# Kernel optimization log

Hardware: AMD Instinct MI355X
Metric: run time of the kernel (lower is better)

The kernel has to match this reference:

```python
import jax, jax.numpy as jnp
import numpy as np

N = 20000      # nodes
E = 320000     # edges
IN = 300       # input_channel
HID = 100      # hidden_channel (= heads*out_channels with heads=1)
R = 50         # num_relations
B = 8          # num_bases (the 4th positional arg 'heads'=8 lands on num_bases in PyG RGATConv)
HEADS = 1
CLS = 3
Q = 64         # number of query (aspect) nodes
EPS = 1e-16


def setup_inputs() -> dict:
    key = jax.random.key(0)
    ks = jax.random.split(key, 16)
    x = jax.random.normal(ks[0], (N, IN), jnp.float32)
    edge_index = jax.random.randint(ks[1], (2, E), 0, N)
    edge_type = jax.random.randint(ks[2], (E,), 0, R)
    query_indices = jax.random.randint(ks[3], (Q,), 0, N)

    def w(k, shape, scale):
        return jax.random.normal(k, shape, jnp.float32) * scale

    comp1 = w(ks[4], (R, B), 0.3)
    basis1 = w(ks[5], (B, IN, HEADS * HID), 1.0 / np.sqrt(IN))
    q1 = w(ks[6], (HEADS * HID, HEADS), 0.1)
    k1 = w(ks[7], (HEADS * HID, HEADS), 0.1)
    b1 = jnp.zeros((HEADS * HID,), jnp.float32)
    comp2 = w(ks[8], (R, B), 0.3)
    basis2 = w(ks[9], (B, HID, HEADS * HID), 1.0 / np.sqrt(HID))
    q2 = w(ks[10], (HEADS * HID, HEADS), 0.1)
    k2 = w(ks[11], (HEADS * HID, HEADS), 0.1)
    b2 = jnp.zeros((HEADS * HID,), jnp.float32)
    Wl = w(ks[12], (CLS, HID), 1.0 / np.sqrt(HID))
    bl = jnp.zeros((CLS,), jnp.float32)
    return dict(x=x, edge_index=edge_index, edge_type=edge_type,
                query_indices=query_indices,
                comp1=comp1, basis1=basis1, q1=q1, k1=k1, b1=b1,
                comp2=comp2, basis2=basis2, q2=q2, k2=k2, b2=b2,
                Wl=Wl, bl=bl)


def segment_softmax(alpha, seg, num_segments):
    # numerically-stable softmax over edges grouped by destination node
    m = jax.ops.segment_max(alpha, seg, num_segments=num_segments)  # [N, H]
    e = jnp.exp(alpha - m[seg])
    s = jax.ops.segment_sum(e, seg, num_segments=num_segments)
    return e / (s[seg] + EPS)


def rgat_conv(x, edge_index, edge_type, comp, basis, q, k, b):
    # basis-decomposed per-relation weight: [R, in, H*out]
    W = jnp.einsum('rb,bio->rio', comp, basis)
    # transform every node under every relation once, then gather per edge
    xt = jnp.einsum('ni,rio->nro', x, W)          # [N, R, H*out]
    src, dst = edge_index[0], edge_index[1]        # j -> i (source_to_target)
    xi = xt[dst, edge_type]                        # [E, H*out]
    xj = xt[src, edge_type]                        # [E, H*out]
    qi = xi @ q                                    # [E, H]
    kj = xj @ k                                    # [E, H]
    alpha = jax.nn.leaky_relu(qi + kj, 0.2)        # additive self-attention
    alpha = segment_softmax(alpha, dst, N)         # across-relation softmax
    msg = xj.reshape(E, HEADS, HID) * alpha[:, :, None]
    out = jax.ops.segment_sum(msg, dst, num_segments=N)  # [N, H, out]
    return out.reshape(N, HEADS * HID) + b         # concat=True


def reference(x, edge_index, edge_type, query_indices,
              comp1, basis1, q1, k1, b1,
              comp2, basis2, q2, k2, b2, Wl, bl):
    h = jax.nn.relu(rgat_conv(x, edge_index, edge_type, comp1, basis1, q1, k1, b1))
    h = jax.nn.relu(rgat_conv(h, edge_index, edge_type, comp2, basis2, q2, k2, b2))
    pooled = h[query_indices].mean(axis=0)          # [HID]
    return pooled @ Wl.T + bl                       # [CLS]
```

## Files before the change

### kernel.cpp

```cpp
#include <hip/hip_runtime.h>
#include <math.h>

#define N_NODES 20000
#define E_EDGES 320000
#define IN_CH   300
#define HID     100
#define R_REL   50
#define NB      8
#define CLS     3
#define NQ      64
#define OUTW    800
#define ZW      128
#define KP1     320
#define KP2     128
#define MPAD    20224
#define NPAIR   79
#define GEMM_RG 25
#define SCAN_BLKS ((N_NODES + 255) / 256)

typedef unsigned short ushort_t;
typedef __attribute__((ext_vector_type(8))) short     short8;
typedef __attribute__((ext_vector_type(8))) unsigned short ushort8;
typedef __attribute__((ext_vector_type(4))) float     f32x4;
typedef __attribute__((ext_vector_type(2))) float     f32x2;

__device__ __forceinline__ ushort_t f2bf_rne(float f) {
    unsigned u = __float_as_uint(f);
    unsigned r = (u + 0x7fffu + ((u >> 16) & 1u)) >> 16;
    return (ushort_t)r;
}
__device__ __forceinline__ float bf2f(ushort_t u) {
    return __uint_as_float((unsigned)u << 16);
}

__global__ __launch_bounds__(256) void zero_deg2(int* __restrict__ dd,
                                                 int* __restrict__ ds) {
    int i = blockIdx.x * 256 + threadIdx.x;
    if (i < N_NODES) { dd[i] = 0; ds[i] = 0; }
}

__global__ __launch_bounds__(256) void hist2_kernel(
        const int* __restrict__ ei, int* __restrict__ dd,
        int* __restrict__ ds) {
    int e = blockIdx.x * 256 + threadIdx.x;
    if (e < E_EDGES) {
        atomicAdd(&dd[ei[E_EDGES + e]], 1);
        atomicAdd(&ds[ei[e]], 1);
    }
}

__global__ __launch_bounds__(256) void scan1_both(
        const int* __restrict__ deg_d, int* __restrict__ rp_d, int* __restrict__ bsum_d,
        const int* __restrict__ deg_s, int* __restrict__ rp_s, int* __restrict__ bsum_s) {
    int set = blockIdx.x / SCAN_BLKS, blk = blockIdx.x % SCAN_BLKS;
    const int* deg = set ? deg_s : deg_d;
    int* rowptr    = set ? rp_s  : rp_d;
    int* bsum      = set ? bsum_s : bsum_d;
    __shared__ int s[256];
    int tid = threadIdx.x;
    int idx = blk * 256 + tid;
    int v = (idx < N_NODES) ? deg[idx] : 0;
    s[tid] = v; __syncthreads();
    #pragma unroll
    for (int off = 1; off < 256; off <<= 1) {
        int t = (tid >= off) ? s[tid - off] : 0;
        __syncthreads();
        s[tid] += t;
        __syncthreads();
    }
    if (idx < N_NODES) rowptr[idx] = s[tid] - v;
    if (tid == 255) bsum[blk] = s[255];
}

__global__ __launch_bounds__(128) void scan2_both(
        int* __restrict__ bsum_d, int* __restrict__ rp_d,
        int* __restrict__ bsum_s, int* __restrict__ rp_s) {
    int* bsum   = blockIdx.x ? bsum_s : bsum_d;
    int* rowptr = blockIdx.x ? rp_s   : rp_d;
    __shared__ int s[128];
    int tid = threadIdx.x;
    int v = (tid < SCAN_BLKS) ? bsum[tid] : 0;
    s[tid] = v; __syncthreads();
    #pragma unroll
    for (int off = 1; off < 128; off <<= 1) {
        int t = (tid >= off) ? s[tid - off] : 0;
        __syncthreads();
        s[tid] += t;
        __syncthreads();
    }
    if (tid < SCAN_BLKS) bsum[tid] = s[tid] - v;
    if (tid == 0) rowptr[N_NODES] = E_EDGES;
}

__global__ __launch_bounds__(256) void scan3_both(
        int* __restrict__ rp_d, const int* __restrict__ bsum_d, int* __restrict__ cur_d,
        int* __restrict__ rp_s, const int* __restrict__ bsum_s, int* __restrict__ cur_s) {
    int set = blockIdx.x / SCAN_BLKS, blk = blockIdx.x % SCAN_BLKS;
    int* rowptr      = set ? rp_s   : rp_d;
    const int* bsum  = set ? bsum_s : bsum_d;
    int* cursor      = set ? cur_s  : cur_d;
    int idx = blk * 256 + threadIdx.x;
    if (idx < N_NODES) {
        int v = rowptr[idx] + bsum[blk];
        rowptr[idx] = v;
        cursor[idx] = v;
    }
}

__global__ __launch_bounds__(256) void scatter_both(
        const int* __restrict__ ei, const int* __restrict__ et,
        int* __restrict__ cur_d, int* __restrict__ cur_s,
        int* __restrict__ skey, int* __restrict__ skey_s,
        int* __restrict__ zidx) {
    int e = blockIdx.x * 256 + threadIdx.x;
    if (e >= E_EDGES) return;
    int s = ei[e], d = ei[E_EDGES + e], rt = et[e];
    int p = atomicAdd(&cur_d[d], 1);
    skey[p] = (s << 6) | rt;
    int qp = atomicAdd(&cur_s[s], 1);
    skey_s[qp] = rt;
    zidx[p] = qp;
}

__global__ __launch_bounds__(256) void split_bt_both(
        const float* __restrict__ basis1, ushort_t* __restrict__ Bt1,
        const float* __restrict__ basis2, ushort_t* __restrict__ Bt2) {
    int idx = blockIdx.x * 256 + threadIdx.x;
    const int n1 = OUTW * KP1;
    if (idx < n1) {
        int n = idx / KP1, k = idx - n * KP1;
        int b = n / HID, o = n - b * HID;
        float v = (k < IN_CH) ? basis1[((size_t)b * IN_CH + k) * HID + o] : 0.f;
        Bt1[idx] = f2bf_rne(v);
    } else {
        int i2 = idx - n1;
        if (i2 >= OUTW * KP2) return;
        int n = i2 / KP2, k = i2 - n * KP2;
        int b = n / HID, o = n - b * HID;
        float v = (k < HID) ? basis2[((size_t)b * HID + k) * HID + o] : 0.f;
        Bt2[i2] = f2bf_rne(v);
    }
}

template<int K, int KP, int RELU>
__global__ __launch_bounds__(256) void cvt_pad_bf16(
        const float* __restrict__ in, ushort_t* __restrict__ out, int M) {
    constexpr int CH = KP / 8;
    int idx = blockIdx.x * 256 + threadIdx.x;
    if (idx >= MPAD * CH) return;
    int n = idx / CH, c = idx - n * CH;
    int k = c * 8;
    float v[8];
    if (n < M && k + 8 <= K) {
        float4 f0 = *(const float4*)&in[(size_t)n * K + k];
        float4 f1 = *(const float4*)&in[(size_t)n * K + k + 4];
        v[0]=f0.x; v[1]=f0.y; v[2]=f0.z; v[3]=f0.w;
        v[4]=f1.x; v[5]=f1.y; v[6]=f1.z; v[7]=f1.w;
    } else {
        #pragma unroll
        for (int i = 0; i < 8; i++)
            v[i] = (n < M && k + i < K) ? in[(size_t)n * K + k + i] : 0.f;
    }
    if (RELU) {
        #pragma unroll
        for (int i = 0; i < 8; i++) v[i] = fmaxf(v[i], 0.f);
    }
    ushort8 hv;
    #pragma unroll
    for (int i = 0; i < 8; i++) hv[i] = f2bf_rne(v[i]);
    *(ushort8*)&out[(size_t)n * KP + k] = hv;
}

template<int KP>
__global__ __launch_bounds__(512, 2) void gemm_mfma(
        const ushort_t* __restrict__ Ab, const ushort_t* __restrict__ Bt,
        ushort_t* __restrict__ xbh, int M) {
    constexpr int KSTEPS = KP / 32;
    constexpr int SW = KP + 8;
    constexpr int CH = KP / 8;
    __shared__ ushort_t Bs[80 * SW];
    int tid = threadIdx.x, lane = tid & 63, wave = tid >> 6;
    int ml = lane & 15, quad = lane >> 4;
    int cb = blockIdx.x / GEMM_RG;
    int rg = blockIdx.x - cb * GEMM_RG;
    int col0 = cb * 80;

    for (int t = tid; t < 80 * CH; t += 512) {
        int c = t / CH, ch = t - c * CH;
        *(ushort8*)&Bs[c * SW + ch * 8] =
            *(const ushort8*)&Bt[(size_t)(col0 + c) * KP + ch * 8];
    }
    __syncthreads();

    const ushort_t* bb = &Bs[(size_t)ml * SW + quad * 8];

    for (int g = rg; g < NPAIR; g += GEMM_RG) {
        int rbase = g * 256 + wave * 32;
        const ushort_t* ar0 = Ab + (size_t)(rbase + ml) * KP + quad * 8;
        const ushort_t* ar1 = ar0 + (size_t)16 * KP;
        short8 a0[KSTEPS], a1[KSTEPS];
        #pragma unroll
        for (int ks = 0; ks < KSTEPS; ks++) {
            a0[ks] = *(const short8*)(ar0 + ks * 32);
            a1[ks] = *(const short8*)(ar1 + ks * 32);
        }
        f32x4 acc0[5] = {}, acc1[5] = {};
        #pragma unroll
        for (int ks = 0; ks < KSTEPS; ks++) {
            short8 bf[5];
            #pragma unroll
            for (int nt = 0; nt < 5; nt++)
                bf[nt] = *(const short8*)(bb + nt * 16 * SW + ks * 32);
            #pragma unroll
            for (int nt = 0; nt < 5; nt++) {
                acc0[nt] = __builtin_amdgcn_mfma_f32_16x16x32_bf16(
                               a0[ks], bf[nt], acc0[nt], 0, 0, 0);
                acc1[nt] = __builtin_amdgcn_mfma_f32_16x16x32_bf16(
                               a1[ks], bf[nt], acc1[nt], 0, 0, 0);
            }
        }
        #pragma unroll
        for (int nt = 0; nt < 5; nt++) {
            #pragma unroll
            for (int r = 0; r < 4; r++) {
                int g0 = rbase + quad * 4 + r;
                if (g0 < M)
                    xbh[(size_t)g0 * OUTW + col0 + nt * 16 + ml] =
                        f2bf_rne(acc0[nt][r]);
                int g1 = g0 + 16;
                if (g1 < M)
                    xbh[(size_t)g1 * OUTW + col0 + nt * 16 + ml] =
                        f2bf_rne(acc1[nt][r]);
            }
        }
    }
}

__global__ __launch_bounds__(256) void qk3_kernel(
        const ushort_t* __restrict__ xbh, const float* __restrict__ q,
        const float* __restrict__ k, float* __restrict__ xbq,
        float* __restrict__ xbk) {
    __shared__ float sq[HID], sk[HID];
    int tid = threadIdx.x;
    if (tid < HID) { sq[tid] = q[tid]; sk[tid] = k[tid]; }
    __syncthreads();
    int idx = blockIdx.x * 256 + tid;
    if (idx >= N_NODES * NB) return;
    const ushort_t* xr = xbh + (size_t)(idx >> 3) * OUTW + (idx & 7) * HID;
    float aq = 0.f, ak = 0.f;
    #pragma unroll
    for (int c = 0; c < 25; c++) {
        ushort4 v = *(const ushort4*)&xr[c * 4];
        #pragma unroll
        for (int i = 0; i < 4; i++) {
            float f = bf2f(((const ushort_t*)&v)[i]);
            aq = fmaf(f, sq[c * 4 + i], aq);
            ak = fmaf(f, sk[c * 4 + i], ak);
        }
    }
    xbq[idx] = aq;
    xbk[idx] = ak;
}

__global__ __launch_bounds__(256) void compute_z(
        const int* __restrict__ rowptr_s, const int* __restrict__ skey_s,
        const float* __restrict__ comp, const ushort_t* __restrict__ xbh,
        ushort_t* __restrict__ Z) {
    __shared__ float scomp[R_REL * NB];
    int tid = threadIdx.x;
    for (int i = tid; i < R_REL * NB; i += 256) scomp[i] = comp[i];
    __syncthreads();
    int wave = tid >> 6, lane = tid & 63;
    int s = blockIdx.x * 4 + wave;
    if (s >= N_NODES) return;
    int beg = rowptr_s[s], end = rowptr_s[s + 1];
    if (beg == end) return;
    int eg = lane >> 4, c16 = lane & 15;
    int cbase = c16 * 8;
    float xr[NB][8];
    #pragma unroll
    for (int b = 0; b < NB; b++)
        #pragma unroll
        for (int i = 0; i < 8; i++) xr[b][i] = 0.f;
    if (cbase < HID) {
        #pragma unroll
        for (int b = 0; b < NB; b++) {
            const ushort_t* base = xbh + (size_t)s * OUTW + b * HID + cbase;
            ushort4 v0 = *(const ushort4*)base;
            xr[b][0] = bf2f(v0.x); xr[b][1] = bf2f(v0.y);
            xr[b][2] = bf2f(v0.z); xr[b][3] = bf2f(v0.w);
            if (cbase + 8 <= HID) {
                ushort4 v1 = *(const ushort4*)(base + 4);
                xr[b][4] = bf2f(v1.x); xr[b][5] = bf2f(v1.y);
                xr[b][6] = bf2f(v1.z); xr[b][7] = bf2f(v1.w);
            }
        }
    }
    for (int w0 = beg; w0 < end; w0 += 64) {
        int kw = (w0 + lane < end) ? skey_s[w0 + lane] : 0;
        int wend = w0 + 64 < end ? w0 + 64 : end;
        for (int p0 = w0; p0 < wend; p0 += 4) {
            int j = p0 - w0 + eg;
            int rt = __shfl(kw, j) & 63;
            int p = p0 + eg;
            const float* cr = &scomp[rt * NB];
            float z[8] = {};
            #pragma unroll
            for (int b = 0; b < NB; b++) {
                float cb = cr[b];
                #pragma unroll
                for (int i = 0; i < 8; i++) z[i] = fmaf(cb, xr[b][i], z[i]);
            }
            ushort8 zz;
            #pragma unroll
            for (int i = 0; i < 8; i++) zz[i] = f2bf_rne(z[i]);
            if (p < end)
                *(ushort8*)&Z[(size_t)p * ZW + cbase] = zz;
        }
    }
}

__global__ __launch_bounds__(256) void msg_soft(
        const int* __restrict__ rowptr, const int* __restrict__ skey,
        const int* __restrict__ zidx,
        const float* __restrict__ comp, const ushort_t* __restrict__ Z,
        const float* __restrict__ xbq, const float* __restrict__ xbk,
        const float* __restrict__ bias, float* __restrict__ h) {
    __shared__ float scomp[R_REL * NB];
    int tid = threadIdx.x;
    for (int i = tid; i < R_REL * NB; i += 256) scomp[i] = comp[i];
    __syncthreads();
    int wave = tid >> 6, lane = tid & 63;
    int d = blockIdx.x * 4 + wave;
    if (d >= N_NODES) return;
    int beg = rowptr[d], end = rowptr[d + 1];

    float4 qd0 = *(const float4*)&xbq[d * NB];
    float4 qd1 = *(const float4*)&xbq[d * NB + 4];

    int l5 = lane & 31;
    bool act = l5 < 25;
    int oc = l5 * 4;
    f32x4 acc = {0.f, 0.f, 0.f, 0.f};
    float m = -1e30f, l = 0.f;

    for (int c0 = beg; c0 < end; c0 += 64) {
        int p = c0 + lane;
        bool valid = p < end;
        float a = -1e30f;
        int zi = 0;
        if (valid) {
            int key = skey[p];
            zi = zidx[p];
            int s = key >> 6, rt = key & 63;
            const float4 c0v = *(const float4*)&scomp[rt * NB];
            const float4 c1v = *(const float4*)&scomp[rt * NB + 4];
            const float4 k0v = *(const float4*)&xbk[s * NB];
            const float4 k1v = *(const float4*)&xbk[s * NB + 4];
            float qi = c0v.x*qd0.x + c0v.y*qd0.y + c0v.z*qd0.z + c0v.w*qd0.w
                     + c1v.x*qd1.x + c1v.y*qd1.y + c1v.z*qd1.z + c1v.w*qd1.w;
            float kj = c0v.x*k0v.x + c0v.y*k0v.y + c0v.z*k0v.z + c0v.w*k0v.w
                     + c1v.x*k1v.x + c1v.y*k1v.y + c1v.z*k1v.z + c1v.w*k1v.w;
            a = qi + kj;
            a = a > 0.f ? a : 0.2f * a;
        }
        float cm = a;
        #pragma unroll
        for (int off = 32; off; off >>= 1) cm = fmaxf(cm, __shfl_xor(cm, off));
        float M = fmaxf(m, cm);
        float scale = __expf(m - M);
        acc *= scale; l *= scale; m = M;
        float wgt = valid ? __expf(a - M) : 0.f;
        float cs = wgt;
        #pragma unroll
        for (int off = 32; off; off >>= 1) cs += __shfl_xor(cs, off);
        l += cs;
        int cnt = end - c0; if (cnt > 64) cnt = 64;
        for (int j = 0; j < cnt; j += 2) {
            int jj = j + (lane >> 5);
            float wj = __shfl(wgt, jj);
            int   zj = __shfl(zi, jj);
            if (act) {
                ushort4 zz = *(const ushort4*)&Z[(size_t)zj * ZW + oc];
                acc.x = fmaf(wj, bf2f(zz.x), acc.x);
                acc.y = fmaf(wj, bf2f(zz.y), acc.y);
                acc.z = fmaf(wj, bf2f(zz.z), acc.z);
                acc.w = fmaf(wj, bf2f(zz.w), acc.w);
            }
        }
    }
    #pragma unroll
    for (int i = 0; i < 4; i++) acc[i] += __shfl_xor(acc[i], 32);
    if (lane < 25) {
        float inv = 1.f / (l + 1e-16f);
        float4 r;
        r.x = bias[oc]     + acc.x * inv;
        r.y = bias[oc + 1] + acc.y * inv;
        r.z = bias[oc + 2] + acc.z * inv;
        r.w = bias[oc + 3] + acc.w * inv;
        *(float4*)&h[(size_t)d * HID + oc] = r;
    }
}

__global__ __launch_bounds__(128) void head_kernel(
        const float* __restrict__ h2, const int* __restrict__ qidx,
        const float* __restrict__ Wl, const float* __restrict__ bl,
        float* __restrict__ out) {
    __shared__ float pooled[HID];
    int tid = threadIdx.x;
    if (tid < HID) {
        float s = 0.f;
        for (int i = 0; i < NQ; i++)
            s += fmaxf(h2[(size_t)qidx[i] * HID + tid], 0.f);
        pooled[tid] = s * (1.0f / NQ);
    }
    __syncthreads();
    if (tid < CLS) {
        float s = bl[tid];
        for (int o = 0; o < HID; o++) s = fmaf(pooled[o], Wl[tid * HID + o], s);
        out[tid] = s;
    }
}

extern "C" void kernel_launch(void* const* d_in, const int* in_sizes, int n_in,
                              void* d_out, int out_size, void* d_ws, size_t ws_size,
                              hipStream_t stream) {
    const float* x      = (const float*)d_in[0];
    const int*   ei     = (const int*)  d_in[1];
    const int*   et     = (const int*)  d_in[2];
    const int*   qidx   = (const int*)  d_in[3];
    const float* comp1  = (const float*)d_in[4];
    const float* basis1 = (const float*)d_in[5];
    const float* q1     = (const float*)d_in[6];
    const float* k1     = (const float*)d_in[7];
    const float* b1     = (const float*)d_in[8];
    const float* comp2  = (const float*)d_in[9];
    const float* basis2 = (const float*)d_in[10];
    const float* q2     = (const float*)d_in[11];
    const float* k2     = (const float*)d_in[12];
    const float* b2     = (const float*)d_in[13];
    const float* Wl     = (const float*)d_in[14];
    const float* bl     = (const float*)d_in[15];
    float* out = (float*)d_out;

    char* w = (char*)d_ws;
    size_t off = 0;
    auto alloc = [&](size_t nbytes) {
        void* p = (void*)(w + off);
        off += ((nbytes + 255) / 256) * 256;
        return p;
    };
    ushort_t* xbh    = (ushort_t*)alloc((size_t)N_NODES * OUTW * 2);
    ushort_t* Z      = (ushort_t*)alloc((size_t)E_EDGES * ZW * 2);
    float*    h1     = (float*)alloc((size_t)N_NODES * HID * 4);
    float*    h2     = (float*)alloc((size_t)N_NODES * HID * 4);
    ushort_t* Bt1    = (ushort_t*)alloc((size_t)OUTW * KP1 * 2);
    ushort_t* Bt2    = (ushort_t*)alloc((size_t)OUTW * KP2 * 2);
    ushort_t* xbA    = (ushort_t*)alloc((size_t)MPAD * KP1 * 2);
    ushort_t* hbA    = (ushort_t*)alloc((size_t)MPAD * KP2 * 2);
    float*    xbq    = (float*)alloc((size_t)N_NODES * NB * 4);
    float*    xbk    = (float*)alloc((size_t)N_NODES * NB * 4);
    int*      deg_d  = (int*)alloc(N_NODES * 4);
    int*      deg_s  = (int*)alloc(N_NODES * 4);
    int*      rp_d   = (int*)alloc((N_NODES + 1) * 4);
    int*      rp_s   = (int*)alloc((N_NODES + 1) * 4);
    int*      cur_d  = (int*)alloc(N_NODES * 4);
    int*      cur_s  = (int*)alloc(N_NODES * 4);
    int*      bsum_d = (int*)alloc(SCAN_BLKS * 4);
    int*      bsum_s = (int*)alloc(SCAN_BLKS * 4);
    int*      skey   = (int*)alloc(E_EDGES * 4);
    int*      skey_s = (int*)alloc(E_EDGES * 4);
    int*      zidx   = (int*)alloc(E_EDGES * 4);

    zero_deg2<<<SCAN_BLKS, 256, 0, stream>>>(deg_d, deg_s);
    hist2_kernel<<<(E_EDGES + 255) / 256, 256, 0, stream>>>(ei, deg_d, deg_s);
    scan1_both<<<2 * SCAN_BLKS, 256, 0, stream>>>(deg_d, rp_d, bsum_d, deg_s, rp_s, bsum_s);
    scan2_both<<<2, 128, 0, stream>>>(bsum_d, rp_d, bsum_s, rp_s);
    scan3_both<<<2 * SCAN_BLKS, 256, 0, stream>>>(rp_d, bsum_d, cur_d, rp_s, bsum_s, cur_s);
    scatter_both<<<(E_EDGES + 255) / 256, 256, 0, stream>>>(ei, et, cur_d, cur_s, skey, skey_s, zidx);
    split_bt_both<<<(OUTW * (KP1 + KP2) + 255) / 256, 256, 0, stream>>>(basis1, Bt1, basis2, Bt2);
    cvt_pad_bf16<IN_CH, KP1, 0><<<(MPAD * (KP1 / 8) + 255) / 256, 256, 0, stream>>>(x, xbA, N_NODES);

    gemm_mfma<KP1><<<10 * GEMM_RG, 512, 0, stream>>>(xbA, Bt1, xbh, N_NODES);
    qk3_kernel<<<(N_NODES * NB + 255) / 256, 256, 0, stream>>>(xbh, q1, k1, xbq, xbk);
    compute_z<<<(N_NODES + 3) / 4, 256, 0, stream>>>(rp_s, skey_s, comp1, xbh, Z);
    msg_soft<<<(N_NODES + 3) / 4, 256, 0, stream>>>(rp_d, skey, zidx, comp1, Z, xbq, xbk, b1, h1);

    cvt_pad_bf16<HID, KP2, 1><<<(MPAD * (KP2 / 8) + 255) / 256, 256, 0, stream>>>(h1, hbA, N_NODES);
    gemm_mfma<KP2><<<10 * GEMM_RG, 512, 0, stream>>>(hbA, Bt2, xbh, N_NODES);
    qk3_kernel<<<(N_NODES * NB + 255) / 256, 256, 0, stream>>>(xbh, q2, k2, xbq, xbk);
    compute_z<<<(N_NODES + 3) / 4, 256, 0, stream>>>(rp_s, skey_s, comp2, xbh, Z);
    msg_soft<<<(N_NODES + 3) / 4, 256, 0, stream>>>(rp_d, skey, zidx, comp2, Z, xbq, xbk, b2, h2);

    head_kernel<<<1, 128, 0, stream>>>(h2, qidx, Wl, bl, out);
}
```

Before: 380.0 us.

## Fuse layer-1 ReLU/bf16 packing into msg_soft and remap GEMM blocks across XCDs

The first-layer message kernel now applies ReLU and writes bf16 directly into the padded GEMM input buffer, so the separate fp32 h1 buffer and the convert/pad kernel are gone. The padded buffer is zeroed once by a new kernel, since padding columns and rows are no longer written by the converter. The GEMM grid grows from 25 to 48 row groups per column block, and the block-to-tile mapping is changed so consecutive blocks spread across the 8 XCDs while blocks sharing B columns stay together. The trade-off is an extra zeroing launch and more GEMM blocks with less work each.

```diff
diff --git a/kernel.cpp b/kernel.cpp
--- a/kernel.cpp
+++ b/kernel.cpp
@@ -15,7 +15,7 @@
 #define KP2     128
 #define MPAD    20224
 #define NPAIR   79
-#define GEMM_RG 25
+#define GEMM_RG 48
 #define SCAN_BLKS ((N_NODES + 255) / 256)
 
 typedef unsigned short ushort_t;
@@ -37,6 +37,14 @@
                                                  int* __restrict__ ds) {
     int i = blockIdx.x * 256 + threadIdx.x;
     if (i < N_NODES) { dd[i] = 0; ds[i] = 0; }
+}
+
+__global__ __launch_bounds__(256) void zero_hbA(ushort_t* __restrict__ p) {
+    int i = blockIdx.x * 256 + threadIdx.x;
+    if (i < MPAD * KP2 / 8) {
+        ushort8 z = {};
+        *(ushort8*)&p[(size_t)i * 8] = z;
+    }
 }
 
 __global__ __launch_bounds__(256) void hist2_kernel(
@@ -181,8 +189,10 @@
     __shared__ ushort_t Bs[80 * SW];
     int tid = threadIdx.x, lane = tid & 63, wave = tid >> 6;
     int ml = lane & 15, quad = lane >> 4;
-    int cb = blockIdx.x / GEMM_RG;
-    int rg = blockIdx.x - cb * GEMM_RG;
+    int b = blockIdx.x;
+    int xcd = b & 7, qq = b >> 3;
+    int cb = qq % 10;
+    int rg = xcd + 8 * (qq / 10);
     int col0 = cb * 80;
 
     for (int t = tid; t < 80 * CH; t += 512) {
@@ -320,12 +330,14 @@
     }
 }
 
+template<int WB>
 __global__ __launch_bounds__(256) void msg_soft(
         const int* __restrict__ rowptr, const int* __restrict__ skey,
         const int* __restrict__ zidx,
         const float* __restrict__ comp, const ushort_t* __restrict__ Z,
         const float* __restrict__ xbq, const float* __restrict__ xbk,
-        const float* __restrict__ bias, float* __restrict__ h) {
+        const float* __restrict__ bias, float* __restrict__ h,
+        ushort_t* __restrict__ hb) {
     __shared__ float scomp[R_REL * NB];
     int tid = threadIdx.x;
     for (int i = tid; i < R_REL * NB; i += 256) scomp[i] = comp[i];
@@ -361,8 +373,8 @@
                      + c1v.x*qd1.x + c1v.y*qd1.y + c1v.z*qd1.z + c1v.w*qd1.w;
             float kj = c0v.x*k0v.x + c0v.y*k0v.y + c0v.z*k0v.z + c0v.w*k0v.w
                      + c1v.x*k1v.x + c1v.y*k1v.y + c1v.z*k1v.z + c1v.w*k1v.w;
-            a = qi + kj;
-            a = a > 0.f ? a : 0.2f * a;
+            float av = qi + kj;
+            a = av > 0.f ? av : 0.2f * av;
         }
         float cm = a;
         #pragma unroll
@@ -398,7 +410,16 @@
         r.y = bias[oc + 1] + acc.y * inv;
         r.z = bias[oc + 2] + acc.z * inv;
         r.w = bias[oc + 3] + acc.w * inv;
-        *(float4*)&h[(size_t)d * HID + oc] = r;
+        if (WB) {
+            ushort4 o;
+            o.x = f2bf_rne(fmaxf(r.x, 0.f));
+            o.y = f2bf_rne(fmaxf(r.y, 0.f));
+            o.z = f2bf_rne(fmaxf(r.z, 0.f));
+            o.w = f2bf_rne(fmaxf(r.w, 0.f));
+            *(ushort4*)&hb[(size_t)d * KP2 + oc] = o;
+        } else {
+            *(float4*)&h[(size_t)d * HID + oc] = r;
+        }
     }
 }
 
@@ -452,7 +473,6 @@
     };
     ushort_t* xbh    = (ushort_t*)alloc((size_t)N_NODES * OUTW * 2);
     ushort_t* Z      = (ushort_t*)alloc((size_t)E_EDGES * ZW * 2);
-    float*    h1     = (float*)alloc((size_t)N_NODES * HID * 4);
     float*    h2     = (float*)alloc((size_t)N_NODES * HID * 4);
     ushort_t* Bt1    = (ushort_t*)alloc((size_t)OUTW * KP1 * 2);
     ushort_t* Bt2    = (ushort_t*)alloc((size_t)OUTW * KP2 * 2);
@@ -473,6 +493,7 @@
     int*      zidx   = (int*)alloc(E_EDGES * 4);
 
     zero_deg2<<<SCAN_BLKS, 256, 0, stream>>>(deg_d, deg_s);
+    zero_hbA<<<(MPAD * KP2 / 8 + 255) / 256, 256, 0, stream>>>(hbA);
     hist2_kernel<<<(E_EDGES + 255) / 256, 256, 0, stream>>>(ei, deg_d, deg_s);
     scan1_both<<<2 * SCAN_BLKS, 256, 0, stream>>>(deg_d, rp_d, bsum_d, deg_s, rp_s, bsum_s);
     scan2_both<<<2, 128, 0, stream>>>(bsum_d, rp_d, bsum_s, rp_s);
@@ -484,13 +505,12 @@
     gemm_mfma<KP1><<<10 * GEMM_RG, 512, 0, stream>>>(xbA, Bt1, xbh, N_NODES);
     qk3_kernel<<<(N_NODES * NB + 255) / 256, 256, 0, stream>>>(xbh, q1, k1, xbq, xbk);
     compute_z<<<(N_NODES + 3) / 4, 256, 0, stream>>>(rp_s, skey_s, comp1, xbh, Z);
-    msg_soft<<<(N_NODES + 3) / 4, 256, 0, stream>>>(rp_d, skey, zidx, comp1, Z, xbq, xbk, b1, h1);
-
-    cvt_pad_bf16<HID, KP2, 1><<<(MPAD * (KP2 / 8) + 255) / 256, 256, 0, stream>>>(h1, hbA, N_NODES);
+    msg_soft<1><<<(N_NODES + 3) / 4, 256, 0, stream>>>(rp_d, skey, zidx, comp1, Z, xbq, xbk, b1, (float*)nullptr, hbA);
+
     gemm_mfma<KP2><<<10 * GEMM_RG, 512, 0, stream>>>(hbA, Bt2, xbh, N_NODES);
     qk3_kernel<<<(N_NODES * NB + 255) / 256, 256, 0, stream>>>(xbh, q2, k2, xbq, xbk);
     compute_z<<<(N_NODES + 3) / 4, 256, 0, stream>>>(rp_s, skey_s, comp2, xbh, Z);
-    msg_soft<<<(N_NODES + 3) / 4, 256, 0, stream>>>(rp_d, skey, zidx, comp2, Z, xbq, xbk, b2, h2);
+    msg_soft<0><<<(N_NODES + 3) / 4, 256, 0, stream>>>(rp_d, skey, zidx, comp2, Z, xbq, xbk, b2, h2, (ushort_t*)nullptr);
 
     head_kernel<<<1, 128, 0, stream>>>(h2, qidx, Wl, bl, out);
 }
```

Result: no change. 378.9 us (-0.3%).
